# Performance work log

Measured on AMD Instinct MI355X. Metric: run time of the kernel, lower is better.

## Reference

```python
import jax, jax.numpy as jnp
import numpy as np

EPS = 1e-6  # LayerNorm eps (norm_layer = partial(nn.LayerNorm, eps=1e-6))
B, CIN, HW, P, D, L, H, F = 32, 3, 224, 16, 768, 12, 12, 3072


def _ln(x, w, b):
    m = x.mean(-1, keepdims=True)
    v = jnp.var(x, axis=-1, keepdims=True)
    return (x - m) / jnp.sqrt(v + EPS) * w + b


def setup_inputs() -> dict:
    key = jax.random.key(0)
    ks = jax.random.split(key, 10)
    s = 0.02  # trunc_normal_ std
    N = (HW // P) ** 2
    return {
        "x": jax.random.normal(ks[0], (B, CIN, HW, HW), jnp.float32),
        "conv_w": jax.random.normal(ks[1], (D, CIN, P, P), jnp.float32) * s,
        "conv_b": jnp.zeros((D,), jnp.float32),
        "cls_token": jax.random.normal(ks[2], (1, 1, D), jnp.float32) * s,
        "pos_embed": jax.random.normal(ks[3], (1, N + 1, D), jnp.float32) * s,
        "ln1_w": jnp.ones((L, D), jnp.float32),
        "ln1_b": jnp.zeros((L, D), jnp.float32),
        "qkv_w": jax.random.normal(ks[4], (L, D, 3 * D), jnp.float32) * s,
        "qkv_b": jnp.zeros((L, 3 * D), jnp.float32),
        "proj_w": jax.random.normal(ks[5], (L, D, D), jnp.float32) * s,
        "proj_b": jnp.zeros((L, D), jnp.float32),
        "ln2_w": jnp.ones((L, D), jnp.float32),
        "ln2_b": jnp.zeros((L, D), jnp.float32),
        "fc1_w": jax.random.normal(ks[6], (L, D, F), jnp.float32) * s,
        "fc1_b": jnp.zeros((L, F), jnp.float32),
        "fc2_w": jax.random.normal(ks[7], (L, F, D), jnp.float32) * s,
        "fc2_b": jnp.zeros((L, D), jnp.float32),
        "lnf_w": jnp.ones((D,), jnp.float32),
        "lnf_b": jnp.zeros((D,), jnp.float32),
    }


def _vit(x, conv_w, conv_b, cls_token, pos_embed,
         ln1_w, ln1_b, qkv_w, qkv_b, proj_w, proj_b,
         ln2_w, ln2_b, fc1_w, fc1_b, fc2_w, fc2_b, lnf_w, lnf_b):
    b = x.shape[0]
    nh = HW // P
    dh = D // H
    scale = dh ** (-0.5)
    # Patch embed: stride-P/kernel-P conv == reshape into patches + GEMM.
    # [B,3,H,W] -> [B, nh*nh, 3*P*P] with (c,ph,pw) flatten order matching conv_w.
    p = x.reshape(b, CIN, nh, P, nh, P).transpose(0, 2, 4, 1, 3, 5)
    p = p.reshape(b, nh * nh, CIN * P * P)
    p = p @ conv_w.reshape(D, -1).T + conv_b  # [B, N, D]
    cls = jnp.broadcast_to(cls_token, (b, 1, D))
    h = jnp.concatenate([cls, p], axis=1) + pos_embed  # [B, N+1, D]

    def block(h, prm):
        l1w, l1b, qw, qb, pw, pb, l2w, l2b, f1w, f1b, f2w, f2b = prm
        y = _ln(h, l1w, l1b)
        qkv = (y @ qw + qb).reshape(b, -1, 3, H, dh)
        q, k, v = qkv[:, :, 0], qkv[:, :, 1], qkv[:, :, 2]  # [B,N,H,dh]
        attn = jnp.einsum("bnhd,bmhd->bhnm", q, k) * scale
        attn = jax.nn.softmax(attn, axis=-1)
        o = jnp.einsum("bhnm,bmhd->bnhd", attn, v).reshape(b, -1, D)
        h = h + (o @ pw + pb)
        y = _ln(h, l2w, l2b)
        h = h + (jax.nn.gelu(y @ f1w + f1b, approximate=False) @ f2w + f2b)
        return h, None

    prms = (ln1_w, ln1_b, qkv_w, qkv_b, proj_w, proj_b,
            ln2_w, ln2_b, fc1_w, fc1_b, fc2_w, fc2_b)
    h, _ = jax.lax.scan(block, h, prms)
    h = _ln(h, lnf_w, lnf_b)
    return h[:, 0][None]  # forward(): x.unsqueeze(0) -> [1, B, D]


def reference(x, conv_w, conv_b, cls_token, pos_embed,
              ln1_w, ln1_b, qkv_w, qkv_b, proj_w, proj_b,
              ln2_w, ln2_b, fc1_w, fc1_b, fc2_w, fc2_b, lnf_w, lnf_b):
    return _vit(x, conv_w, conv_b, cls_token, pos_embed,
                ln1_w, ln1_b, qkv_w, qkv_b, proj_w, proj_b,
                ln2_w, ln2_b, fc1_w, fc1_b, fc2_w, fc2_b, lnf_w, lnf_b)
```

## Files before the change

kernel.cpp:

```cpp
#include <hip/hip_runtime.h>
#include <cmath>

typedef __bf16 bf16;
typedef __bf16 bf16x8 __attribute__((ext_vector_type(8)));
typedef __bf16 bf16x4 __attribute__((ext_vector_type(4)));
typedef float  f32x4  __attribute__((ext_vector_type(4)));

#define MFMA16(a,b,c) __builtin_amdgcn_mfma_f32_16x16x32_bf16(a,b,c,0,0,0)

__device__ __forceinline__ void async_ld16(const void* g, void* l) {
  __builtin_amdgcn_global_load_lds((__attribute__((address_space(1))) void*)(g),
                                   (__attribute__((address_space(3))) void*)(l),
                                   16, 0, 0);
}

enum { EPI_PATCH = 0, EPI_BF16 = 1, EPI_RESID = 2, EPI_GELU = 3 };

template <int EPI>
__global__ __launch_bounds__(256) void gemm128(
    const bf16* __restrict__ A, const bf16* __restrict__ Wt,
    const float* __restrict__ bias, bf16* __restrict__ outB,
    float* __restrict__ outF, int M, int N, int K, int Kc)
{
  __shared__ bf16 As[2][128 * 32];
  __shared__ bf16 Bs[2][128 * 32];
  const int tid  = threadIdx.x;
  const int lane = tid & 63, wid = tid >> 6;
  const int qr   = lane & 15, quad = lane >> 4;
  const int wm   = wid >> 1, wn = wid & 1;
  const int bm   = blockIdx.x, bn = blockIdx.y, z = blockIdx.z;
  const int kbeg = z * Kc;
  const int kend = min(K, kbeg + Kc);
  const int sr   = wid * 16 + (lane >> 2);
  const int scol = (lane & 3) * 8;

  f32x4 zero4 = {0.f, 0.f, 0.f, 0.f};
  f32x4 acc[4][4];
#pragma unroll
  for (int i = 0; i < 4; i++)
#pragma unroll
    for (int j = 0; j < 4; j++) acc[i][j] = zero4;

  const int ra0 = min(bm * 128 + sr, M - 1);
  const int ra1 = min(bm * 128 + 64 + sr, M - 1);
  const size_t nr0 = (size_t)(bn * 128 + sr);
  const size_t nr1 = (size_t)(bn * 128 + 64 + sr);

  auto stage = [&](int buf, int k0) {
    async_ld16(A + (size_t)ra0 * K + k0 + scol, &As[buf][(wid * 16) * 32]);
    async_ld16(A + (size_t)ra1 * K + k0 + scol, &As[buf][(64 + wid * 16) * 32]);
    async_ld16(Wt + nr0 * K + k0 + scol, &Bs[buf][(wid * 16) * 32]);
    async_ld16(Wt + nr1 * K + k0 + scol, &Bs[buf][(64 + wid * 16) * 32]);
  };

  stage(0, kbeg);
  __syncthreads();
  int cur = 0;
  for (int k0 = kbeg; k0 < kend; k0 += 32) {
    const int kn = k0 + 32;
    if (kn < kend) stage(cur ^ 1, kn);
    bf16x8 af[4], bfr[4];
#pragma unroll
    for (int mi = 0; mi < 4; mi++)
      af[mi] = *(const bf16x8*)&As[cur][(wm * 64 + mi * 16 + qr) * 32 + quad * 8];
#pragma unroll
    for (int ni = 0; ni < 4; ni++)
      bfr[ni] = *(const bf16x8*)&Bs[cur][(wn * 64 + ni * 16 + qr) * 32 + quad * 8];
#pragma unroll
    for (int mi = 0; mi < 4; mi++)
#pragma unroll
      for (int ni = 0; ni < 4; ni++)
        acc[mi][ni] = MFMA16(af[mi], bfr[ni], acc[mi][ni]);
    __syncthreads();
    cur ^= 1;
  }

#pragma unroll
  for (int mi = 0; mi < 4; mi++) {
#pragma unroll
    for (int ni = 0; ni < 4; ni++) {
      const int row0 = bm * 128 + wm * 64 + mi * 16 + quad * 4;
      const int col  = bn * 128 + wn * 64 + ni * 16 + qr;
      const float bv = (z == 0) ? bias[col] : 0.f;
#pragma unroll
      for (int r = 0; r < 4; r++) {
        const int row = row0 + r;
        if (row < M) {
          float v = acc[mi][ni][r] + bv;
          if constexpr (EPI == EPI_PATCH) {
            int bb = row / 196, nn = row % 196;
            int orow = bb * 197 + 1 + nn;
            atomicAdd(&outF[(size_t)orow * 768 + col], v);
          } else if constexpr (EPI == EPI_BF16) {
            outB[(size_t)row * N + col] = (bf16)v;
          } else if constexpr (EPI == EPI_GELU) {
            float gel = 0.5f * v * (1.f + erff(v * 0.70710678118f));
            outB[(size_t)row * N + col] = (bf16)gel;
          } else {
            atomicAdd(&outF[(size_t)row * 768 + col], v);
          }
        }
      }
    }
  }
}

template <int EPI>
__global__ __launch_bounds__(512, 4) void gemm_bt8(
    const bf16* __restrict__ A, const bf16* __restrict__ Wt,
    const float* __restrict__ bias, bf16* __restrict__ outB,
    int M, int N, int K)
{
  __shared__ bf16 As[2][128 * 32];
  __shared__ bf16 Bs[2][128 * 32];
  const int tid  = threadIdx.x;
  const int lane = tid & 63, wid = tid >> 6;
  const int qr   = lane & 15, quad = lane >> 4;
  const int wm   = wid >> 1, wn = wid & 1;
  const int bm   = blockIdx.x, bn = blockIdx.y;
  const int sr   = wid * 16 + (lane >> 2);
  const int scol = (lane & 3) * 8;

  f32x4 zero4 = {0.f, 0.f, 0.f, 0.f};
  f32x4 acc[2][4];
#pragma unroll
  for (int i = 0; i < 2; i++)
#pragma unroll
    for (int j = 0; j < 4; j++) acc[i][j] = zero4;

  const int ra = min(bm * 128 + sr, M - 1);
  const size_t nr = (size_t)(bn * 128 + sr);

  auto stage = [&](int buf, int k0) {
    async_ld16(A  + (size_t)ra * K + k0 + scol, &As[buf][(wid * 16) * 32]);
    async_ld16(Wt + nr * K + k0 + scol,         &Bs[buf][(wid * 16) * 32]);
  };

  stage(0, 0);
  __syncthreads();
  int cur = 0;
  for (int k0 = 0; k0 < K; k0 += 32) {
    const int kn = k0 + 32;
    if (kn < K) stage(cur ^ 1, kn);
    bf16x8 af[2], bfr[4];
#pragma unroll
    for (int mi = 0; mi < 2; mi++)
      af[mi] = *(const bf16x8*)&As[cur][(wm * 32 + mi * 16 + qr) * 32 + quad * 8];
#pragma unroll
    for (int ni = 0; ni < 4; ni++)
      bfr[ni] = *(const bf16x8*)&Bs[cur][(wn * 64 + ni * 16 + qr) * 32 + quad * 8];
#pragma unroll
    for (int mi = 0; mi < 2; mi++)
#pragma unroll
      for (int ni = 0; ni < 4; ni++)
        acc[mi][ni] = MFMA16(af[mi], bfr[ni], acc[mi][ni]);
    __syncthreads();
    cur ^= 1;
  }

#pragma unroll
  for (int mi = 0; mi < 2; mi++) {
#pragma unroll
    for (int ni = 0; ni < 4; ni++) {
      const int row0 = bm * 128 + wm * 32 + mi * 16 + quad * 4;
      const int col  = bn * 128 + wn * 64 + ni * 16 + qr;
      const float bv = bias[col];
#pragma unroll
      for (int r = 0; r < 4; r++) {
        const int row = row0 + r;
        if (row < M) {
          float v = acc[mi][ni][r] + bv;
          if constexpr (EPI == EPI_GELU) {
            float gel = 0.5f * v * (1.f + erff(v * 0.70710678118f));
            outB[(size_t)row * N + col] = (bf16)gel;
          } else {
            outB[(size_t)row * N + col] = (bf16)v;
          }
        }
      }
    }
  }
}

__global__ __launch_bounds__(256) void attn_kernel(
    const bf16* __restrict__ qkv, bf16* __restrict__ o)
{
  __shared__ __align__(16) char smem[68864];
  bf16 (*Qs)[72]  = (bf16(*)[72])(smem);
  bf16 (*Ks)[72]  = (bf16(*)[72])(smem + 9216);
  bf16 (*Ps)[232] = (bf16(*)[232])(smem + 9216);
  bf16 (*Vt)[232] = (bf16(*)[232])(smem + 39168);

  const int tid  = threadIdx.x;
  const int lane = tid & 63, wid = tid >> 6;
  const int qr   = lane & 15, quad = lane >> 4;
  const int qt   = blockIdx.x & 3, bh = blockIdx.x >> 2;
  const int head = bh % 12, b = bh / 12;
  const int q0   = qt * 64;
  const size_t base = (size_t)b * 197 * 2304 + head * 64;

  {
    int r = tid >> 2, cb = (tid & 3) * 16;
    int s = q0 + r; if (s > 196) s = 196;
    const bf16* src = qkv + base + (size_t)s * 2304 + cb;
    *(uint4*)&Qs[r][cb]     = *(const uint4*)src;
    *(uint4*)&Qs[r][cb + 8] = *(const uint4*)(src + 8);
  }
  for (int rr = tid >> 2; rr < 208; rr += 64) {
    int cb = (tid & 3) * 16;
    uint4 v0 = make_uint4(0, 0, 0, 0), v1 = make_uint4(0, 0, 0, 0);
    if (rr < 197) {
      const bf16* src = qkv + base + 768 + (size_t)rr * 2304 + cb;
      v0 = *(const uint4*)src; v1 = *(const uint4*)(src + 8);
    }
    *(uint4*)&Ks[rr][cb] = v0; *(uint4*)&Ks[rr][cb + 8] = v1;
  }
  for (int rr = tid >> 2; rr < 224; rr += 64) {
    int cb = (tid & 3) * 16;
    bf16 tmp[16];
    if (rr < 197) {
      const bf16* src = qkv + base + 1536 + (size_t)rr * 2304 + cb;
      *(uint4*)&tmp[0] = *(const uint4*)src;
      *(uint4*)&tmp[8] = *(const uint4*)(src + 8);
    } else {
#pragma unroll
      for (int j = 0; j < 16; j++) tmp[j] = (bf16)0.f;
    }
#pragma unroll
    for (int j = 0; j < 16; j++) Vt[cb + j][rr] = tmp[j];
  }
  __syncthreads();

  bf16x8 qa0 = *(const bf16x8*)&Qs[wid * 16 + qr][quad * 8];
  bf16x8 qa1 = *(const bf16x8*)&Qs[wid * 16 + qr][32 + quad * 8];
  f32x4 zero4 = {0.f, 0.f, 0.f, 0.f};
  f32x4 sc[13];
#pragma unroll
  for (int t = 0; t < 13; t++) sc[t] = zero4;
#pragma unroll
  for (int t = 0; t < 13; t++) {
    bf16x8 kb0 = *(const bf16x8*)&Ks[t * 16 + qr][quad * 8];
    bf16x8 kb1 = *(const bf16x8*)&Ks[t * 16 + qr][32 + quad * 8];
    sc[t] = MFMA16(qa0, kb0, sc[t]);
    sc[t] = MFMA16(qa1, kb1, sc[t]);
  }
  float mx[4] = {-1e30f, -1e30f, -1e30f, -1e30f};
#pragma unroll
  for (int t = 0; t < 13; t++) {
    bool valid = (t * 16 + qr) < 197;
#pragma unroll
    for (int r = 0; r < 4; r++) {
      float v = sc[t][r] * 0.125f;
      sc[t][r] = v;
      if (valid) mx[r] = fmaxf(mx[r], v);
    }
  }
#pragma unroll
  for (int r = 0; r < 4; r++)
#pragma unroll
    for (int off = 1; off < 16; off <<= 1)
      mx[r] = fmaxf(mx[r], __shfl_xor(mx[r], off, 16));
  float sum[4] = {0.f, 0.f, 0.f, 0.f};
#pragma unroll
  for (int t = 0; t < 13; t++) {
    bool valid = (t * 16 + qr) < 197;
#pragma unroll
    for (int r = 0; r < 4; r++) {
      float e = valid ? __expf(sc[t][r] - mx[r]) : 0.f;
      sc[t][r] = e; sum[r] += e;
    }
  }
#pragma unroll
  for (int r = 0; r < 4; r++) {
#pragma unroll
    for (int off = 1; off < 16; off <<= 1)
      sum[r] += __shfl_xor(sum[r], off, 16);
    sum[r] = 1.f / sum[r];
  }
  __syncthreads();
#pragma unroll
  for (int t = 0; t < 13; t++)
#pragma unroll
    for (int r = 0; r < 4; r++)
      Ps[wid * 16 + quad * 4 + r][t * 16 + qr] = (bf16)(sc[t][r] * sum[r]);
  {
    bf16x4 zz = {(bf16)0.f, (bf16)0.f, (bf16)0.f, (bf16)0.f};
    *(bf16x4*)&Ps[wid * 16 + qr][208 + quad * 4] = zz;
  }
  __syncthreads();

  f32x4 oa[4];
#pragma unroll
  for (int ni = 0; ni < 4; ni++) oa[ni] = zero4;
#pragma unroll
  for (int k0 = 0; k0 < 224; k0 += 32) {
    bf16x8 pa = *(const bf16x8*)&Ps[wid * 16 + qr][k0 + quad * 8];
#pragma unroll
    for (int ni = 0; ni < 4; ni++) {
      bf16x8 vb = *(const bf16x8*)&Vt[ni * 16 + qr][k0 + quad * 8];
      oa[ni] = MFMA16(pa, vb, oa[ni]);
    }
  }
#pragma unroll
  for (int ni = 0; ni < 4; ni++)
#pragma unroll
    for (int r = 0; r < 4; r++) {
      int row = q0 + wid * 16 + quad * 4 + r;
      if (row < 197)
        o[(((size_t)b * 197 + row) * 12 + head) * 64 + ni * 16 + qr] =
            (bf16)oa[ni][r];
    }
}

__global__ __launch_bounds__(256) void ln_bf16(
    const float* __restrict__ h, const float* __restrict__ w,
    const float* __restrict__ b, bf16* __restrict__ y, int rows)
{
  int row = blockIdx.x * 4 + (threadIdx.x >> 6);
  int lane = threadIdx.x & 63;
  if (row >= rows) return;
  const float* hr = h + (size_t)row * 768;
  float v[12]; float s = 0.f;
#pragma unroll
  for (int i = 0; i < 12; i++) { v[i] = hr[lane + 64 * i]; s += v[i]; }
#pragma unroll
  for (int off = 32; off >= 1; off >>= 1) s += __shfl_xor(s, off, 64);
  float mean = s * (1.f / 768.f);
  float q = 0.f;
#pragma unroll
  for (int i = 0; i < 12; i++) { float d = v[i] - mean; q += d * d; }
#pragma unroll
  for (int off = 32; off >= 1; off >>= 1) q += __shfl_xor(q, off, 64);
  float rstd = rsqrtf(q * (1.f / 768.f) + 1e-6f);
  bf16* yr = y + (size_t)row * 768;
#pragma unroll
  for (int i = 0; i < 12; i++)
    yr[lane + 64 * i] = (bf16)((v[i] - mean) * rstd * w[lane + 64 * i] + b[lane + 64 * i]);
}

__global__ __launch_bounds__(256) void ln_final(
    const float* __restrict__ h, const float* __restrict__ w,
    const float* __restrict__ b, float* __restrict__ out)
{
  int bi = blockIdx.x * 4 + (threadIdx.x >> 6);
  int lane = threadIdx.x & 63;
  if (bi >= 32) return;
  const float* hr = h + (size_t)bi * 197 * 768;
  float v[12]; float s = 0.f;
#pragma unroll
  for (int i = 0; i < 12; i++) { v[i] = hr[lane + 64 * i]; s += v[i]; }
#pragma unroll
  for (int off = 32; off >= 1; off >>= 1) s += __shfl_xor(s, off, 64);
  float mean = s * (1.f / 768.f);
  float q = 0.f;
#pragma unroll
  for (int i = 0; i < 12; i++) { float d = v[i] - mean; q += d * d; }
#pragma unroll
  for (int off = 32; off >= 1; off >>= 1) q += __shfl_xor(q, off, 64);
  float rstd = rsqrtf(q * (1.f / 768.f) + 1e-6f);
#pragma unroll
  for (int i = 0; i < 12; i++)
    out[(size_t)bi * 768 + lane + 64 * i] =
        (v[i] - mean) * rstd * w[lane + 64 * i] + b[lane + 64 * i];
}

__global__ __launch_bounds__(256) void transpose_w(
    const float* __restrict__ in, bf16* __restrict__ out, int R, int C)
{
  __shared__ float t[32][33];
  size_t zoff = (size_t)blockIdx.z * R * C;
  in += zoff; out += zoff;
  int c0 = blockIdx.x * 32, r0 = blockIdx.y * 32;
  int lx = threadIdx.x & 31, ly = threadIdx.x >> 5;
#pragma unroll
  for (int i = 0; i < 32; i += 8) t[ly + i][lx] = in[(size_t)(r0 + ly + i) * C + c0 + lx];
  __syncthreads();
#pragma unroll
  for (int i = 0; i < 32; i += 8)
    out[(size_t)(c0 + ly + i) * R + r0 + lx] = (bf16)t[lx][ly + i];
}

__global__ __launch_bounds__(256) void convert_bf16(
    const float* __restrict__ in, bf16* __restrict__ out, int n)
{
  int i = blockIdx.x * 256 + threadIdx.x;
  if (i < n) out[i] = (bf16)in[i];
}

__global__ __launch_bounds__(256) void patch_extract(
    const float* __restrict__ x, bf16* __restrict__ patches)
{
  int i = blockIdx.x * 256 + threadIdx.x;
  if (i >= 6272 * 192) return;
  int m = i / 192, kq = (i % 192) * 4;
  int b = m / 196, pp = m % 196, py = pp / 14, px = pp % 14;
  int c = kq >> 8, rem = kq & 255, iy = rem >> 4, ix = rem & 15;
  const float4 v = *(const float4*)&x[(((size_t)(b * 3 + c) * 224 + py * 16 + iy) * 224) + px * 16 + ix];
  bf16x4 pv = {(bf16)v.x, (bf16)v.y, (bf16)v.z, (bf16)v.w};
  *(bf16x4*)&patches[(size_t)m * 768 + kq] = pv;
}

__global__ __launch_bounds__(256) void h_init_full(
    const float* __restrict__ cls, const float* __restrict__ pos,
    float* __restrict__ h)
{
  int i = blockIdx.x * 256 + threadIdx.x;
  if (i >= 6304 * 192) return;
  int row = i / 192, c4 = (i % 192) * 4;
  int s = row % 197;
  float4 pv = *(const float4*)&pos[(size_t)s * 768 + c4];
  if (s == 0) {
    float4 cv = *(const float4*)&cls[c4];
    pv.x += cv.x; pv.y += cv.y; pv.z += cv.z; pv.w += cv.w;
  }
  *(float4*)&h[(size_t)row * 768 + c4] = pv;
}

extern "C" void kernel_launch(void* const* d_in, const int* in_sizes, int n_in,
                              void* d_out, int out_size, void* d_ws, size_t ws_size,
                              hipStream_t stream)
{
  const float* x      = (const float*)d_in[0];
  const float* conv_w = (const float*)d_in[1];
  const float* conv_b = (const float*)d_in[2];
  const float* cls    = (const float*)d_in[3];
  const float* pos    = (const float*)d_in[4];
  const float* ln1_w  = (const float*)d_in[5];
  const float* ln1_b  = (const float*)d_in[6];
  const float* qkv_w  = (const float*)d_in[7];
  const float* qkv_b  = (const float*)d_in[8];
  const float* proj_w = (const float*)d_in[9];
  const float* proj_b = (const float*)d_in[10];
  const float* ln2_w  = (const float*)d_in[11];
  const float* ln2_b  = (const float*)d_in[12];
  const float* fc1_w  = (const float*)d_in[13];
  const float* fc1_b  = (const float*)d_in[14];
  const float* fc2_w  = (const float*)d_in[15];
  const float* fc2_b  = (const float*)d_in[16];
  const float* lnf_w  = (const float*)d_in[17];
  const float* lnf_b  = (const float*)d_in[18];
  float* out = (float*)d_out;
  (void)in_sizes; (void)n_in; (void)out_size; (void)ws_size;

  char* ws = (char*)d_ws;
  size_t off = 0;
  auto alloc = [&](size_t bytes) -> char* {
    char* p = ws + off;
    off += (bytes + 255) & ~(size_t)255;
    return p;
  };

  bf16*  convwB  = (bf16*)alloc((size_t)768 * 768 * 2);
  bf16*  qkvT    = (bf16*)alloc((size_t)12 * 2304 * 768 * 2);
  bf16*  projT   = (bf16*)alloc((size_t)12 * 768 * 768 * 2);
  bf16*  fc1T    = (bf16*)alloc((size_t)12 * 3072 * 768 * 2);
  bf16*  fc2T    = (bf16*)alloc((size_t)12 * 768 * 3072 * 2);
  bf16*  patches = (bf16*)alloc((size_t)6272 * 768 * 2);
  float* h       = (float*)alloc((size_t)6304 * 768 * 4);
  bf16*  y       = (bf16*)alloc((size_t)6304 * 768 * 2);
  bf16*  qkvB    = (bf16*)alloc((size_t)6304 * 2304 * 2);
  bf16*  obuf    = (bf16*)alloc((size_t)6304 * 768 * 2);
  bf16*  g       = (bf16*)alloc((size_t)6304 * 3072 * 2);

  convert_bf16<<<(768 * 768 + 255) / 256, 256, 0, stream>>>(conv_w, convwB, 768 * 768);
  transpose_w<<<dim3(2304 / 32, 768 / 32, 12), 256, 0, stream>>>(qkv_w, qkvT, 768, 2304);
  transpose_w<<<dim3(768 / 32, 768 / 32, 12), 256, 0, stream>>>(proj_w, projT, 768, 768);
  transpose_w<<<dim3(3072 / 32, 768 / 32, 12), 256, 0, stream>>>(fc1_w, fc1T, 768, 3072);
  transpose_w<<<dim3(768 / 32, 3072 / 32, 12), 256, 0, stream>>>(fc2_w, fc2T, 3072, 768);

  patch_extract<<<(6272 * 192) / 256, 256, 0, stream>>>(x, patches);
  h_init_full<<<(6304 * 192 + 255) / 256, 256, 0, stream>>>(cls, pos, h);
  gemm128<EPI_PATCH><<<dim3(49, 6, 2), 256, 0, stream>>>(
      patches, convwB, conv_b, nullptr, h, 6272, 768, 768, 384);

  for (int l = 0; l < 12; l++) {
    ln_bf16<<<1576, 256, 0, stream>>>(h, ln1_w + l * 768, ln1_b + l * 768, y, 6304);
    gemm_bt8<EPI_BF16><<<dim3(50, 18), 512, 0, stream>>>(
        y, qkvT + (size_t)l * 2304 * 768, qkv_b + l * 2304, qkvB,
        6304, 2304, 768);
    attn_kernel<<<32 * 12 * 4, 256, 0, stream>>>(qkvB, obuf);
    gemm128<EPI_RESID><<<dim3(50, 6, 2), 256, 0, stream>>>(
        obuf, projT + (size_t)l * 768 * 768, proj_b + l * 768, nullptr, h,
        6304, 768, 768, 384);
    ln_bf16<<<1576, 256, 0, stream>>>(h, ln2_w + l * 768, ln2_b + l * 768, y, 6304);
    gemm_bt8<EPI_GELU><<<dim3(50, 24), 512, 0, stream>>>(
        y, fc1T + (size_t)l * 3072 * 768, fc1_b + l * 3072, g,
        6304, 3072, 768);
    gemm128<EPI_RESID><<<dim3(50, 6, 2), 256, 0, stream>>>(
        g, fc2T + (size_t)l * 768 * 3072, fc2_b + l * 768, nullptr, h,
        6304, 768, 3072, 1536);
  }
  ln_final<<<8, 256, 0, stream>>>(h, lnf_w, lnf_b, out);
}
```

Before: 3.749 ms.

## Triple-buffer GEMM LDS staging with explicit vmcnt waits and MFMA priority

Both GEMM kernels move from a double-buffered to a three-stage LDS ring. Two tiles stay in flight ahead of compute, and each stage waits only for its own tile using partial s_waitcnt vmcnt counts rather than a full drain. The MFMA block is raised with s_setprio to favour math issue over loads. The aim is to hide global-load latency better, at the cost of 50% more LDS per block, which may reduce occupancy. The hand-counted vmcnt values also assume the outstanding loads are exactly the issued stages, and the tile count must be at least 3.

```diff
diff --git a/kernel.cpp b/kernel.cpp
--- a/kernel.cpp
+++ b/kernel.cpp
@@ -22,8 +22,8 @@
     const float* __restrict__ bias, bf16* __restrict__ outB,
     float* __restrict__ outF, int M, int N, int K, int Kc)
 {
-  __shared__ bf16 As[2][128 * 32];
-  __shared__ bf16 Bs[2][128 * 32];
+  __shared__ bf16 As[3][128 * 32];
+  __shared__ bf16 Bs[3][128 * 32];
   const int tid  = threadIdx.x;
   const int lane = tid & 63, wid = tid >> 6;
   const int qr   = lane & 15, quad = lane >> 4;
@@ -53,26 +53,37 @@
     async_ld16(Wt + nr1 * K + k0 + scol, &Bs[buf][(64 + wid * 16) * 32]);
   };
 
-  stage(0, kbeg);
-  __syncthreads();
-  int cur = 0;
-  for (int k0 = kbeg; k0 < kend; k0 += 32) {
-    const int kn = k0 + 32;
-    if (kn < kend) stage(cur ^ 1, kn);
+  const int nt = (kend - kbeg) >> 5;
+  stage(0, kbeg); stage(1, kbeg + 32); stage(2, kbeg + 64);
+  int buf = 0;
+  for (int t = 0; t < nt; ++t) {
+    if (t + 2 < nt)       asm volatile("s_waitcnt vmcnt(8)" ::: "memory");
+    else if (t + 1 < nt)  asm volatile("s_waitcnt vmcnt(4)" ::: "memory");
+    else                  asm volatile("s_waitcnt vmcnt(0)" ::: "memory");
+    __builtin_amdgcn_s_barrier();
+    asm volatile("" ::: "memory");
     bf16x8 af[4], bfr[4];
+    const bf16* Ab = &As[buf][0];
+    const bf16* Bb = &Bs[buf][0];
 #pragma unroll
     for (int mi = 0; mi < 4; mi++)
-      af[mi] = *(const bf16x8*)&As[cur][(wm * 64 + mi * 16 + qr) * 32 + quad * 8];
+      af[mi] = *(const bf16x8*)&Ab[(wm * 64 + mi * 16 + qr) * 32 + quad * 8];
 #pragma unroll
     for (int ni = 0; ni < 4; ni++)
-      bfr[ni] = *(const bf16x8*)&Bs[cur][(wn * 64 + ni * 16 + qr) * 32 + quad * 8];
+      bfr[ni] = *(const bf16x8*)&Bb[(wn * 64 + ni * 16 + qr) * 32 + quad * 8];
+    __builtin_amdgcn_s_setprio(1);
 #pragma unroll
     for (int mi = 0; mi < 4; mi++)
 #pragma unroll
       for (int ni = 0; ni < 4; ni++)
         acc[mi][ni] = MFMA16(af[mi], bfr[ni], acc[mi][ni]);
-    __syncthreads();
-    cur ^= 1;
+    __builtin_amdgcn_s_setprio(0);
+    __builtin_amdgcn_sched_barrier(0);
+    asm volatile("" ::: "memory");
+    __builtin_amdgcn_s_barrier();
+    asm volatile("" ::: "memory");
+    if (t + 3 < nt) stage(buf, kbeg + (t + 3) * 32);
+    buf = (buf == 2) ? 0 : buf + 1;
   }
 
 #pragma unroll
@@ -111,8 +122,8 @@
     const float* __restrict__ bias, bf16* __restrict__ outB,
     int M, int N, int K)
 {
-  __shared__ bf16 As[2][128 * 32];
-  __shared__ bf16 Bs[2][128 * 32];
+  __shared__ bf16 As[3][128 * 32];
+  __shared__ bf16 Bs[3][128 * 32];
   const int tid  = threadIdx.x;
   const int lane = tid & 63, wid = tid >> 6;
   const int qr   = lane & 15, quad = lane >> 4;
@@ -136,26 +147,37 @@
     async_ld16(Wt + nr * K + k0 + scol,         &Bs[buf][(wid * 16) * 32]);
   };
 
-  stage(0, 0);
-  __syncthreads();
-  int cur = 0;
-  for (int k0 = 0; k0 < K; k0 += 32) {
-    const int kn = k0 + 32;
-    if (kn < K) stage(cur ^ 1, kn);
+  const int nt = K >> 5;
+  stage(0, 0); stage(1, 32); stage(2, 64);
+  int buf = 0;
+  for (int t = 0; t < nt; ++t) {
+    if (t + 2 < nt)       asm volatile("s_waitcnt vmcnt(4)" ::: "memory");
+    else if (t + 1 < nt)  asm volatile("s_waitcnt vmcnt(2)" ::: "memory");
+    else                  asm volatile("s_waitcnt vmcnt(0)" ::: "memory");
+    __builtin_amdgcn_s_barrier();
+    asm volatile("" ::: "memory");
     bf16x8 af[2], bfr[4];
+    const bf16* Ab = &As[buf][0];
+    const bf16* Bb = &Bs[buf][0];
 #pragma unroll
     for (int mi = 0; mi < 2; mi++)
-      af[mi] = *(const bf16x8*)&As[cur][(wm * 32 + mi * 16 + qr) * 32 + quad * 8];
+      af[mi] = *(const bf16x8*)&Ab[(wm * 32 + mi * 16 + qr) * 32 + quad * 8];
 #pragma unroll
     for (int ni = 0; ni < 4; ni++)
-      bfr[ni] = *(const bf16x8*)&Bs[cur][(wn * 64 + ni * 16 + qr) * 32 + quad * 8];
+      bfr[ni] = *(const bf16x8*)&Bb[(wn * 64 + ni * 16 + qr) * 32 + quad * 8];
+    __builtin_amdgcn_s_setprio(1);
 #pragma unroll
     for (int mi = 0; mi < 2; mi++)
 #pragma unroll
       for (int ni = 0; ni < 4; ni++)
         acc[mi][ni] = MFMA16(af[mi], bfr[ni], acc[mi][ni]);
-    __syncthreads();
-    cur ^= 1;
+    __builtin_amdgcn_s_setprio(0);
+    __builtin_amdgcn_sched_barrier(0);
+    asm volatile("" ::: "memory");
+    __builtin_amdgcn_s_barrier();
+    asm volatile("" ::: "memory");
+    if (t + 3 < nt) stage(buf, (t + 3) * 32);
+    buf = (buf == 2) ? 0 : buf + 1;
   }
 
 #pragma unroll
```

After: 3.733 ms. Within noise of the previous version (-0.4%).
